# Kernel optimization log

Measured on AMD Instinct MI355X. Metric: run time of the kernel, lower is better.

## Reference

```python
import jax, jax.numpy as jnp
import numpy as np

N_NODES = 100000
N_EDGES = 1600000
IN_CH = 128
NHIDDEN = 64
OUT_CH = 40
NLAYERS = 4
ALPHA = 0.1


def setup_inputs() -> dict:
    key = jax.random.key(0)
    ks = jax.random.split(key, 7)
    x = jax.random.normal(ks[0], (N_NODES, IN_CH), dtype=jnp.float32)
    edge_index = jax.random.randint(ks[1], (2, N_EDGES), 0, N_NODES, dtype=jnp.int64)
    batch_graph = jnp.zeros((N_NODES,), dtype=jnp.int64)
    fc1_w = jax.random.normal(ks[2], (NHIDDEN, IN_CH), dtype=jnp.float32) * (1.0 / np.sqrt(IN_CH))
    fc1_b = jax.random.normal(ks[3], (NHIDDEN,), dtype=jnp.float32) * 0.01
    conv_w = jax.random.normal(ks[4], (NLAYERS, NHIDDEN, NHIDDEN), dtype=jnp.float32) * (1.0 / np.sqrt(NHIDDEN))
    fc2_w = jax.random.normal(ks[5], (OUT_CH, NHIDDEN), dtype=jnp.float32) * (1.0 / np.sqrt(NHIDDEN))
    fc2_b = jax.random.normal(ks[6], (OUT_CH,), dtype=jnp.float32) * 0.01
    return {"x": x, "edge_index": edge_index, "batch_graph": batch_graph,
            "fc1_w": fc1_w, "fc1_b": fc1_b, "conv_w": conv_w,
            "fc2_w": fc2_w, "fc2_b": fc2_b}


def reference(x, edge_index, batch_graph, fc1_w, fc1_b, conv_w, fc2_w, fc2_b):
    # eval mode: dropout layers are identity
    n = x.shape[0]
    row, col = edge_index[0], edge_index[1]  # source, target

    # gcn_norm with add_self_loops=False: sym deg^-1/2 normalization
    deg = jax.ops.segment_sum(jnp.ones_like(row, dtype=x.dtype), col, num_segments=n)
    dinv = jnp.where(deg > 0, deg ** -0.5, 0.0)
    norm = (dinv[row] * dinv[col])[:, None]  # [E, 1]

    h = jax.nn.relu(x @ fc1_w.T + fc1_b)  # [N, nhidden]
    h0 = h
    nlayers = conv_w.shape[0]
    for i in range(nlayers):
        # GCN2Conv: aggregate, initial-residual mix, weight1 matmul (beta=1)
        agg = jax.ops.segment_sum(h[row] * norm, col, num_segments=n)
        mixed = (1.0 - ALPHA) * agg + ALPHA * h0
        h = jax.nn.relu(mixed @ conv_w[i])
    out = h @ fc2_w.T + fc2_b  # [N, out_channels]
    return out
```

## Files before the change

### kernel.cpp

```cpp
#include <hip/hip_runtime.h>
#include <hip/hip_fp16.h>

#define N_NODES 100000
#define N_EDGES 1600000
#define IN_CH   128
#define NHID    64
#define OUT_CH  40
#define NBLK    391
#define NBUCK   196
#define BCAP    8960
#define ECAP    1024


__global__ __launch_bounds__(256) void k_scan1(const int* __restrict__ cnt,
                                               int* __restrict__ rowptr,
                                               int* __restrict__ bsum) {
    __shared__ int s[256];
    int t = threadIdx.x;
    int n = blockIdx.x * 256 + t;
    int v = (n < N_NODES) ? cnt[n] : 0;
    s[t] = v;
    __syncthreads();
    for (int off = 1; off < 256; off <<= 1) {
        int add = (t >= off) ? s[t - off] : 0;
        __syncthreads();
        s[t] += add;
        __syncthreads();
    }
    int incl = s[t];
    if (n < N_NODES) rowptr[n] = incl - v;
    if (t == 255) bsum[blockIdx.x] = incl;
}

__global__ __launch_bounds__(512) void k_scan2(int* __restrict__ bsum) {
    __shared__ int s[512];
    int t = threadIdx.x;
    int v = (t < NBLK) ? bsum[t] : 0;
    s[t] = v;
    __syncthreads();
    for (int off = 1; off < 512; off <<= 1) {
        int add = (t >= off) ? s[t - off] : 0;
        __syncthreads();
        s[t] += add;
        __syncthreads();
    }
    if (t < NBLK) bsum[t] = s[t] - v;
}

__global__ __launch_bounds__(256) void k_scan3(const int* __restrict__ cnt,
                                               const int* __restrict__ bsum,
                                               int* __restrict__ rowptr,
                                               float* __restrict__ dinv) {
    int n = blockIdx.x * 256 + threadIdx.x;
    if (n < N_NODES) {
        int rp = rowptr[n] + bsum[n >> 8];
        rowptr[n] = rp;
        int c = cnt[n];
        dinv[n] = (c > 0) ? rsqrtf((float)c) : 0.0f;
    }
    if (blockIdx.x == 0 && threadIdx.x == 0) rowptr[N_NODES] = N_EDGES;
}


__global__ __launch_bounds__(256) void k_scatA(const int* __restrict__ ei,
                                               int* __restrict__ bucketCnt,
                                               int2* __restrict__ ebufA) {
    __shared__ int hist[NBUCK];
    __shared__ int base[NBUCK];
    int t = threadIdx.x;
    int chunk = blockIdx.x * 4096;
    for (int i = t; i < NBUCK; i += 256) hist[i] = 0;
    __syncthreads();
#pragma unroll 4
    for (int i = 0; i < 16; i++) {
        int e = chunk + i * 256 + t;
        if (e < N_EDGES) atomicAdd(&hist[ei[N_EDGES + e] >> 9], 1);
    }
    __syncthreads();
    for (int b = t; b < NBUCK; b += 256) {
        int h = hist[b];
        base[b] = h ? atomicAdd(&bucketCnt[b], h) : 0;
    }
    __syncthreads();
#pragma unroll 4
    for (int i = 0; i < 16; i++) {
        int e = chunk + i * 256 + t;
        if (e < N_EDGES) {
            int r = ei[e], c = ei[N_EDGES + e];
            int pos = atomicAdd(&base[c >> 9], 1);
            ebufA[(size_t)(c >> 9) * BCAP + pos] = make_int2(r, c);
        }
    }
}


__global__ __launch_bounds__(256) void k_deg(const int2* __restrict__ ebufA,
                                             const int* __restrict__ bucketCnt,
                                             int* __restrict__ cnt) {
    __shared__ int hist[512];
    int b = blockIdx.x;
    int nodeB = b * 512;
    int t = threadIdx.x;
    for (int i = t; i < 512; i += 256) hist[i] = 0;
    __syncthreads();
    int nE = bucketCnt[b];
    const int2* src = ebufA + (size_t)b * BCAP;
    for (int i = t; i < nE; i += 256) atomicAdd(&hist[src[i].y - nodeB], 1);
    __syncthreads();
    for (int i = t; i < 512; i += 256) {
        int node = nodeB + i;
        if (node < N_NODES) cnt[node] = hist[i];
    }
}


__global__ __launch_bounds__(256) void k_scatB(const int2* __restrict__ ebufA,
                                               const int* __restrict__ bucketCnt,
                                               const float* __restrict__ dinv,
                                               const int* __restrict__ rowptr,
                                               int2* __restrict__ e8) {
    __shared__ int lcur[512];
    int b = blockIdx.x;
    int nodeB = b * 512;
    int t = threadIdx.x;
    for (int i = t; i < 512; i += 256) {
        int node = nodeB + i;
        lcur[i] = (node < N_NODES) ? rowptr[node] : 0;
    }
    __syncthreads();
    int nE = bucketCnt[b];
    const int2* src = ebufA + (size_t)b * BCAP;
    for (int i = t; i < nE; i += 256) {
        int2 rc = src[i];
        float w = dinv[rc.x] * dinv[rc.y];
        int pos = atomicAdd(&lcur[rc.y - nodeB], 1);
        e8[pos] = make_int2(rc.x, __float_as_int(w));
    }
}

__device__ __forceinline__ void store_h4(__half* dst, float a, float b, float c, float d) {
    union { uint2 u; __half2 h[2]; } pk;
    pk.h[0] = __floats2half2_rn(a, b);
    pk.h[1] = __floats2half2_rn(c, d);
    *(uint2*)dst = pk.u;
}


__global__ __launch_bounds__(256, 4) void k_fc1(const float* __restrict__ x,
                                                const float* __restrict__ w,
                                                const float* __restrict__ b,
                                                __half* __restrict__ h016) {
    __shared__ float xs[64 * 128];
    int t = threadIdx.x;
    int nodeBase = blockIdx.x * 64;

    {
        int lane8 = t & 7, rhalf = t >> 3;
#pragma unroll
        for (int r2 = 0; r2 < 2; r2++) {
            int nl = r2 * 32 + rhalf;
            int n = nodeBase + nl;
            int swz = (nl ^ (nl >> 3)) & 7;
            float4* dstrow = (float4*)(xs + nl * 128);
            if (n < N_NODES) {
                const float4* src = (const float4*)(x + (size_t)n * IN_CH);
#pragma unroll
                for (int q = 0; q < 4; q++) dstrow[(q * 8 + lane8) ^ swz] = src[q * 8 + lane8];
            } else {
                float4 z = {0.f, 0.f, 0.f, 0.f};
#pragma unroll
                for (int q = 0; q < 4; q++) dstrow[(q * 8 + lane8) ^ swz] = z;
            }
        }
    }
    __syncthreads();

    int tx = t & 15, ty = t >> 4;
    int n0 = tx * 4, o0 = ty * 4;
    int swz0 = ((n0 + 0) ^ ((n0 + 0) >> 3)) & 7;
    int swz1 = ((n0 + 1) ^ ((n0 + 1) >> 3)) & 7;
    int swz2 = ((n0 + 2) ^ ((n0 + 2) >> 3)) & 7;
    int swz3 = ((n0 + 3) ^ ((n0 + 3) >> 3)) & 7;
    const float4* xrow0 = (const float4*)(xs + (n0 + 0) * 128);
    const float4* xrow1 = (const float4*)(xs + (n0 + 1) * 128);
    const float4* xrow2 = (const float4*)(xs + (n0 + 2) * 128);
    const float4* xrow3 = (const float4*)(xs + (n0 + 3) * 128);

    float c[4][4];
#pragma unroll
    for (int i = 0; i < 4; i++)
#pragma unroll
        for (int j = 0; j < 4; j++) c[i][j] = 0.f;

#pragma unroll 4
    for (int k = 0; k < IN_CH; k += 4) {
        int kk = k >> 2;
        float4 b0 = *(const float4*)&w[(size_t)(o0 + 0) * IN_CH + k];
        float4 b1 = *(const float4*)&w[(size_t)(o0 + 1) * IN_CH + k];
        float4 b2 = *(const float4*)&w[(size_t)(o0 + 2) * IN_CH + k];
        float4 b3 = *(const float4*)&w[(size_t)(o0 + 3) * IN_CH + k];
        float4 a0 = xrow0[kk ^ swz0];
        float4 a1 = xrow1[kk ^ swz1];
        float4 a2 = xrow2[kk ^ swz2];
        float4 a3 = xrow3[kk ^ swz3];
#pragma unroll
        for (int i = 0; i < 4; i++) {
            float4 a = (i == 0) ? a0 : (i == 1) ? a1 : (i == 2) ? a2 : a3;
            c[i][0] = fmaf(a.x, b0.x, fmaf(a.y, b0.y, fmaf(a.z, b0.z, fmaf(a.w, b0.w, c[i][0]))));
            c[i][1] = fmaf(a.x, b1.x, fmaf(a.y, b1.y, fmaf(a.z, b1.z, fmaf(a.w, b1.w, c[i][1]))));
            c[i][2] = fmaf(a.x, b2.x, fmaf(a.y, b2.y, fmaf(a.z, b2.z, fmaf(a.w, b2.w, c[i][2]))));
            c[i][3] = fmaf(a.x, b3.x, fmaf(a.y, b3.y, fmaf(a.z, b3.z, fmaf(a.w, b3.w, c[i][3]))));
        }
    }

    float4 bias = *(const float4*)&b[o0];
#pragma unroll
    for (int i = 0; i < 4; i++) {
        int n = nodeBase + n0 + i;
        if (n < N_NODES) {
            store_h4(&h016[(size_t)n * NHID + o0],
                     fmaxf(c[i][0] + bias.x, 0.f), fmaxf(c[i][1] + bias.y, 0.f),
                     fmaxf(c[i][2] + bias.z, 0.f), fmaxf(c[i][3] + bias.w, 0.f));
        }
    }
}


__global__ __launch_bounds__(256, 4) void k_conv(const __half* __restrict__ hin,
                                                 const __half* __restrict__ h0f16,
                                                 const int* __restrict__ rowptr,
                                                 const int2* __restrict__ e8,
                                                 const float* __restrict__ W,
                                                 __half* __restrict__ hout) {
    __shared__ int2  eS[ECAP];
    __shared__ float mix[32 * 68];
    int t = threadIdx.x;
    int nodeBase = blockIdx.x * 32;
    int grp = t >> 3;
    int cg = (t & 7) * 8;

    int base0 = rowptr[nodeBase];
    int nE = rowptr[nodeBase + 32] - base0;
    int nStage = (nE < ECAP) ? nE : ECAP;
    for (int i = t; i < nStage; i += 256) eS[i] = e8[base0 + i];

    int n = nodeBase + grp;
    int s = rowptr[n], e = rowptr[n + 1];
    int d = e - s;
    int hi = (d > 0) ? (e - 1) : 0;
    __syncthreads();

    float acc[8];
#pragma unroll
    for (int i = 0; i < 8; i++) acc[i] = 0.f;

#define LOADM(pm, jb)                                                    \
    {                                                                    \
        _Pragma("unroll")                                                \
        for (int u = 0; u < 4; u++) {                                    \
            int idx = min((jb) + u, hi);                                 \
            int li = idx - base0;                                        \
            if (li < ECAP) pm[u] = eS[li];                               \
            else           pm[u] = e8[idx];                              \
        }                                                                \
    }
#define ISSUE(pv, pm)                                                    \
    {                                                                    \
        _Pragma("unroll")                                                \
        for (int u = 0; u < 4; u++)                                      \
            pv[u] = *(const float4*)&hin[(size_t)pm[u].x * NHID + cg];   \
    }
#define FMA4(pm, pv, jb)                                                 \
    {                                                                    \
        _Pragma("unroll")                                                \
        for (int u = 0; u < 4; u++) {                                    \
            float wgt = ((jb) + u < e) ? __int_as_float(pm[u].y) : 0.f;  \
            const __half* hp = (const __half*)&pv[u];                    \
            _Pragma("unroll")                                            \
            for (int q = 0; q < 8; q++)                                  \
                acc[q] = fmaf(wgt, __half2float(hp[q]), acc[q]);         \
        }                                                                \
    }

    int2  pmA[4], pmB[4], pmC[4];
    float4 pvA[4], pvB[4], pvC[4];
    if (d > 0) {
        LOADM(pmA, s);     ISSUE(pvA, pmA);
        LOADM(pmB, s + 4); ISSUE(pvB, pmB);
        LOADM(pmC, s + 8); ISSUE(pvC, pmC);
    }

    for (int j = s; j < e; j += 12) {
        {
            FMA4(pmA, pvA, j);
            int jn = j + 12;
            if (jn < e) { LOADM(pmA, jn); ISSUE(pvA, pmA); }
        }
        if (j + 4 < e) {
            FMA4(pmB, pvB, j + 4);
            int jn = j + 16;
            if (jn < e) { LOADM(pmB, jn); ISSUE(pvB, pmB); }
        }
        if (j + 8 < e) {
            FMA4(pmC, pvC, j + 8);
            int jn = j + 20;
            if (jn < e) { LOADM(pmC, jn); ISSUE(pvC, pmC); }
        }
    }
#undef LOADM
#undef ISSUE
#undef FMA4

    {
        float4 raw = *(const float4*)&h0f16[(size_t)n * NHID + cg];
        const __half* h0h = (const __half*)&raw;
        float m[8];
#pragma unroll
        for (int q = 0; q < 8; q++)
            m[q] = fmaf(0.9f, acc[q], 0.1f * __half2float(h0h[q]));
        float4 m0 = {m[0], m[1], m[2], m[3]};
        float4 m1 = {m[4], m[5], m[6], m[7]};
        *(float4*)&mix[grp * 68 + cg] = m0;
        *(float4*)&mix[grp * 68 + cg + 4] = m1;
    }
    __syncthreads();

    int tx = t & 15, ty = t >> 4;
    int o0 = tx * 4, r0 = ty * 2;
    float c[2][4];
#pragma unroll
    for (int i = 0; i < 2; i++)
#pragma unroll
        for (int j = 0; j < 4; j++) c[i][j] = 0.f;

#pragma unroll 4
    for (int k = 0; k < NHID; k += 4) {
        float4 b0 = *(const float4*)&W[(k + 0) * NHID + o0];
        float4 b1 = *(const float4*)&W[(k + 1) * NHID + o0];
        float4 b2 = *(const float4*)&W[(k + 2) * NHID + o0];
        float4 b3 = *(const float4*)&W[(k + 3) * NHID + o0];
#pragma unroll
        for (int i = 0; i < 2; i++) {
            float4 a = *(const float4*)&mix[(r0 + i) * 68 + k];
            c[i][0] = fmaf(a.x, b0.x, fmaf(a.y, b1.x, fmaf(a.z, b2.x, fmaf(a.w, b3.x, c[i][0]))));
            c[i][1] = fmaf(a.x, b0.y, fmaf(a.y, b1.y, fmaf(a.z, b2.y, fmaf(a.w, b3.y, c[i][1]))));
            c[i][2] = fmaf(a.x, b0.z, fmaf(a.y, b1.z, fmaf(a.z, b2.z, fmaf(a.w, b3.z, c[i][2]))));
            c[i][3] = fmaf(a.x, b0.w, fmaf(a.y, b1.w, fmaf(a.z, b2.w, fmaf(a.w, b3.w, c[i][3]))));
        }
    }
#pragma unroll
    for (int i = 0; i < 2; i++) {
        int n2 = nodeBase + r0 + i;
        store_h4(&hout[(size_t)n2 * NHID + o0],
                 fmaxf(c[i][0], 0.f), fmaxf(c[i][1], 0.f),
                 fmaxf(c[i][2], 0.f), fmaxf(c[i][3], 0.f));
    }
}


__global__ __launch_bounds__(256) void k_fc2(const __half* __restrict__ h,
                                             const float* __restrict__ w,
                                             const float* __restrict__ b,
                                             float* __restrict__ out) {
    __shared__ float wT[NHID * 44];
    __shared__ float hs[64 * 68];
    int t = threadIdx.x;
    int nodeBase = blockIdx.x * 64;

    for (int id = t; id < NHID * OUT_CH; id += 256) {
        int o = id >> 6, k = id & 63;
        wT[k * 44 + o] = w[id];
    }
    {
        int nl = t >> 2, seg = t & 3;
        int n = nodeBase + nl;
        float* dst = hs + nl * 68 + seg * 16;
        if (n < N_NODES) {
            float4 raw0 = *(const float4*)&h[(size_t)n * NHID + seg * 16];
            float4 raw1 = *(const float4*)&h[(size_t)n * NHID + seg * 16 + 8];
            const __half2* hp0 = (const __half2*)&raw0;
            const __half2* hp1 = (const __half2*)&raw1;
#pragma unroll
            for (int q = 0; q < 4; q++) {
                float2 f = __half22float2(hp0[q]);
                dst[q * 2 + 0] = f.x;
                dst[q * 2 + 1] = f.y;
            }
#pragma unroll
            for (int q = 0; q < 4; q++) {
                float2 f = __half22float2(hp1[q]);
                dst[8 + q * 2 + 0] = f.x;
                dst[8 + q * 2 + 1] = f.y;
            }
        } else {
#pragma unroll
            for (int q = 0; q < 16; q++) dst[q] = 0.f;
        }
    }
    __syncthreads();

    if (t < 160) {
        int tx = t % 10, ty = t / 10;
        int o0 = tx * 4, n0 = ty * 4;
        float c[4][4];
#pragma unroll
        for (int i = 0; i < 4; i++)
#pragma unroll
            for (int j = 0; j < 4; j++) c[i][j] = 0.f;

#pragma unroll 4
        for (int k = 0; k < NHID; k += 4) {
            float4 b0 = *(const float4*)&wT[(k + 0) * 44 + o0];
            float4 b1 = *(const float4*)&wT[(k + 1) * 44 + o0];
            float4 b2 = *(const float4*)&wT[(k + 2) * 44 + o0];
            float4 b3 = *(const float4*)&wT[(k + 3) * 44 + o0];
#pragma unroll
            for (int i = 0; i < 4; i++) {
                float4 a = *(const float4*)&hs[(n0 + i) * 68 + k];
                c[i][0] = fmaf(a.x, b0.x, fmaf(a.y, b1.x, fmaf(a.z, b2.x, fmaf(a.w, b3.x, c[i][0]))));
                c[i][1] = fmaf(a.x, b0.y, fmaf(a.y, b1.y, fmaf(a.z, b2.y, fmaf(a.w, b3.y, c[i][1]))));
                c[i][2] = fmaf(a.x, b0.z, fmaf(a.y, b1.z, fmaf(a.z, b2.z, fmaf(a.w, b3.z, c[i][2]))));
                c[i][3] = fmaf(a.x, b0.w, fmaf(a.y, b1.w, fmaf(a.z, b2.w, fmaf(a.w, b3.w, c[i][3]))));
            }
        }
        float4 bias = *(const float4*)&b[o0];
#pragma unroll
        for (int i = 0; i < 4; i++) {
            int n = nodeBase + n0 + i;
            if (n < N_NODES) {
                float4 v;
                v.x = c[i][0] + bias.x;
                v.y = c[i][1] + bias.y;
                v.z = c[i][2] + bias.z;
                v.w = c[i][3] + bias.w;
                *(float4*)&out[(size_t)n * OUT_CH + o0] = v;
            }
        }
    }
}


extern "C" void kernel_launch(void* const* d_in, const int* in_sizes, int n_in,
                              void* d_out, int out_size, void* d_ws, size_t ws_size,
                              hipStream_t stream) {
    const float* x    = (const float*)d_in[0];
    const int*   ei   = (const int*)d_in[1];
    const float* fc1w = (const float*)d_in[3];
    const float* fc1b = (const float*)d_in[4];
    const float* cw   = (const float*)d_in[5];
    const float* fc2w = (const float*)d_in[6];
    const float* fc2b = (const float*)d_in[7];
    float* out = (float*)d_out;

    char* p = (char*)d_ws;
    auto alloc = [&](size_t bytes) { char* r = p; p += (bytes + 255) & ~(size_t)255; return r; };
    __half* h016   = (__half*)alloc((size_t)N_NODES * NHID * 2);
    __half* ha16   = (__half*)alloc((size_t)N_NODES * NHID * 2);
    __half* hb16   = (__half*)alloc((size_t)N_NODES * NHID * 2);
    int2*   e8     = (int2*)  alloc(((size_t)N_EDGES + 8) * 8);
    int2*   ebufA  = (int2*)  alloc((size_t)NBUCK * BCAP * 8);
    int*    cnt    = (int*)   alloc((size_t)N_NODES * 4);
    int*    rowptr = (int*)   alloc((size_t)(N_NODES + 1) * 4);
    int*    bCnt   = (int*)   alloc((size_t)NBUCK * 4);
    float*  dinv   = (float*) alloc((size_t)N_NODES * 4);
    int*    bsum   = (int*)   alloc(512 * 4);

    hipMemsetAsync(bCnt, 0, (size_t)NBUCK * 4, stream);
    k_scatA<<<(N_EDGES + 4095) / 4096, 256, 0, stream>>>(ei, bCnt, ebufA);
    k_deg  <<<NBUCK, 256, 0, stream>>>(ebufA, bCnt, cnt);
    k_scan1<<<NBLK, 256, 0, stream>>>(cnt, rowptr, bsum);
    k_scan2<<<1, 512, 0, stream>>>(bsum);
    k_scan3<<<NBLK, 256, 0, stream>>>(cnt, bsum, rowptr, dinv);
    k_scatB<<<NBUCK, 256, 0, stream>>>(ebufA, bCnt, dinv, rowptr, e8);

    int gb64 = (N_NODES + 63) / 64;
    int gb32 = N_NODES / 32;
    k_fc1 <<<gb64, 256, 0, stream>>>(x, fc1w, fc1b, h016);
    k_conv<<<gb32, 256, 0, stream>>>(h016, h016, rowptr, e8, cw + 0 * NHID * NHID, ha16);
    k_conv<<<gb32, 256, 0, stream>>>(ha16, h016, rowptr, e8, cw + 1 * NHID * NHID, hb16);
    k_conv<<<gb32, 256, 0, stream>>>(hb16, h016, rowptr, e8, cw + 2 * NHID * NHID, ha16);
    k_conv<<<gb32, 256, 0, stream>>>(ha16, h016, rowptr, e8, cw + 3 * NHID * NHID, hb16);
    k_fc2 <<<gb64, 256, 0, stream>>>(hb16, fc2w, fc2b, out);
}
```

Measured before the change: 425.1 us.

## Factor symmetric norm into node scaling and store 4-byte edge indices

Rewrites the normalized aggregation as dinv[dst] times the sum of pre-scaled features, so each node's output is pre-multiplied by dinv[src] when written. Edges then store only the source index (4 bytes instead of 8), and the inner loop becomes plain adds, with padded lanes pointing at a zeroed sentinel row. The prefetch depth drops from three batches of four to two. This halves edge-list traffic and removes per-edge multiplies, but adds an extra fp16 rounding of the scaled features and reuses the bucket buffer for the final layer's output.

New measurement: 441.7 us. +3.9%, slower.

```diff
diff --git a/kernel.cpp b/kernel.cpp
--- a/kernel.cpp
+++ b/kernel.cpp
@@ -116,9 +116,8 @@
 
 __global__ __launch_bounds__(256) void k_scatB(const int2* __restrict__ ebufA,
                                                const int* __restrict__ bucketCnt,
-                                               const float* __restrict__ dinv,
                                                const int* __restrict__ rowptr,
-                                               int2* __restrict__ e8) {
+                                               int* __restrict__ e4) {
     __shared__ int lcur[512];
     int b = blockIdx.x;
     int nodeB = b * 512;
@@ -132,9 +131,8 @@
     const int2* src = ebufA + (size_t)b * BCAP;
     for (int i = t; i < nE; i += 256) {
         int2 rc = src[i];
-        float w = dinv[rc.x] * dinv[rc.y];
         int pos = atomicAdd(&lcur[rc.y - nodeB], 1);
-        e8[pos] = make_int2(rc.x, __float_as_int(w));
+        e4[pos] = rc.x;
     }
 }
 
@@ -149,7 +147,9 @@
 __global__ __launch_bounds__(256, 4) void k_fc1(const float* __restrict__ x,
                                                 const float* __restrict__ w,
                                                 const float* __restrict__ b,
-                                                __half* __restrict__ h016) {
+                                                const float* __restrict__ dinv,
+                                                __half* __restrict__ h016,
+                                                __half* __restrict__ hs1) {
     __shared__ float xs[64 * 128];
     int t = threadIdx.x;
     int nodeBase = blockIdx.x * 64;
@@ -218,106 +218,125 @@
     for (int i = 0; i < 4; i++) {
         int n = nodeBase + n0 + i;
         if (n < N_NODES) {
-            store_h4(&h016[(size_t)n * NHID + o0],
-                     fmaxf(c[i][0] + bias.x, 0.f), fmaxf(c[i][1] + bias.y, 0.f),
-                     fmaxf(c[i][2] + bias.z, 0.f), fmaxf(c[i][3] + bias.w, 0.f));
-        }
-    }
-}
-
-
-__global__ __launch_bounds__(256, 4) void k_conv(const __half* __restrict__ hin,
-                                                 const __half* __restrict__ h0f16,
+            float vx = fmaxf(c[i][0] + bias.x, 0.f);
+            float vy = fmaxf(c[i][1] + bias.y, 0.f);
+            float vz = fmaxf(c[i][2] + bias.z, 0.f);
+            float vw = fmaxf(c[i][3] + bias.w, 0.f);
+            store_h4(&h016[(size_t)n * NHID + o0], vx, vy, vz, vw);
+            float dn = dinv[n];
+            store_h4(&hs1[(size_t)n * NHID + o0], vx * dn, vy * dn, vz * dn, vw * dn);
+        }
+    }
+}
+
+
+__global__ __launch_bounds__(256, 4) void k_conv(const __half* __restrict__ hs,
+                                                 const __half* __restrict__ h0,
                                                  const int* __restrict__ rowptr,
-                                                 const int2* __restrict__ e8,
+                                                 const int* __restrict__ e4,
                                                  const float* __restrict__ W,
-                                                 __half* __restrict__ hout) {
-    __shared__ int2  eS[ECAP];
+                                                 const float* __restrict__ dinv,
+                                                 __half* __restrict__ hout,
+                                                 int scaled) {
+    __shared__ int   eS[ECAP];
     __shared__ float mix[32 * 68];
     int t = threadIdx.x;
     int nodeBase = blockIdx.x * 32;
     int grp = t >> 3;
     int cg = (t & 7) * 8;
 
+    int n = nodeBase + grp;
+    int s = rowptr[n], e = rowptr[n + 1];
     int base0 = rowptr[nodeBase];
     int nE = rowptr[nodeBase + 32] - base0;
     int nStage = (nE < ECAP) ? nE : ECAP;
-    for (int i = t; i < nStage; i += 256) eS[i] = e8[base0 + i];
-
-    int n = nodeBase + grp;
-    int s = rowptr[n], e = rowptr[n + 1];
-    int d = e - s;
-    int hi = (d > 0) ? (e - 1) : 0;
-    __syncthreads();
-
-    float acc[8];
-#pragma unroll
-    for (int i = 0; i < 8; i++) acc[i] = 0.f;
-
+    for (int i = t; i < nStage; i += 256) eS[i] = e4[base0 + i];
+
+#define LOADM_G(pm, jb)                                                  \
+    {                                                                    \
+        _Pragma("unroll")                                                \
+        for (int u = 0; u < 4; u++) {                                    \
+            int idx = (jb) + u;                                          \
+            pm[u] = (idx < e) ? e4[idx] : N_NODES;                       \
+        }                                                                \
+    }
 #define LOADM(pm, jb)                                                    \
     {                                                                    \
         _Pragma("unroll")                                                \
         for (int u = 0; u < 4; u++) {                                    \
-            int idx = min((jb) + u, hi);                                 \
-            int li = idx - base0;                                        \
-            if (li < ECAP) pm[u] = eS[li];                               \
-            else           pm[u] = e8[idx];                              \
+            int idx = (jb) + u;                                          \
+            int m = N_NODES;                                             \
+            if (idx < e) {                                               \
+                int li = idx - base0;                                    \
+                m = (li < ECAP) ? eS[li] : e4[idx];                      \
+            }                                                            \
+            pm[u] = m;                                                   \
         }                                                                \
     }
 #define ISSUE(pv, pm)                                                    \
     {                                                                    \
         _Pragma("unroll")                                                \
         for (int u = 0; u < 4; u++)                                      \
-            pv[u] = *(const float4*)&hin[(size_t)pm[u].x * NHID + cg];   \
-    }
-#define FMA4(pm, pv, jb)                                                 \
+            pv[u] = *(const float4*)&hs[(size_t)pm[u] * NHID + cg];      \
+    }
+#define ACC4(cv)                                                         \
     {                                                                    \
         _Pragma("unroll")                                                \
         for (int u = 0; u < 4; u++) {                                    \
-            float wgt = ((jb) + u < e) ? __int_as_float(pm[u].y) : 0.f;  \
-            const __half* hp = (const __half*)&pv[u];                    \
+            const __half2* hp = (const __half2*)&cv[u];                  \
             _Pragma("unroll")                                            \
-            for (int q = 0; q < 8; q++)                                  \
-                acc[q] = fmaf(wgt, __half2float(hp[q]), acc[q]);         \
+            for (int q = 0; q < 4; q++) {                                \
+                float2 f = __half22float2(hp[q]);                        \
+                acc[q * 2 + 0] += f.x;                                   \
+                acc[q * 2 + 1] += f.y;                                   \
+            }                                                            \
         }                                                                \
     }
 
-    int2  pmA[4], pmB[4], pmC[4];
-    float4 pvA[4], pvB[4], pvC[4];
-    if (d > 0) {
-        LOADM(pmA, s);     ISSUE(pvA, pmA);
-        LOADM(pmB, s + 4); ISSUE(pvB, pmB);
-        LOADM(pmC, s + 8); ISSUE(pvC, pmC);
-    }
-
-    for (int j = s; j < e; j += 12) {
+    int    pmA[4], pmB[4];
+    float4 pvA[4], pvB[4];
+    LOADM_G(pmA, s);     ISSUE(pvA, pmA);
+    LOADM_G(pmB, s + 4); ISSUE(pvB, pmB);
+
+    float dn = dinv[n];
+    float4 h0raw = *(const float4*)&h0[(size_t)n * NHID + cg];
+
+    float acc[8];
+#pragma unroll
+    for (int i = 0; i < 8; i++) acc[i] = 0.f;
+
+    __syncthreads();
+
+    for (int j = s; j < e; j += 8) {
         {
-            FMA4(pmA, pvA, j);
+            float4 cv[4];
+#pragma unroll
+            for (int u = 0; u < 4; u++) cv[u] = pvA[u];
+            int jn = j + 8;
+            if (jn < e) { LOADM(pmA, jn); ISSUE(pvA, pmA); }
+            ACC4(cv);
+        }
+        if (j + 4 < e) {
+            float4 cv[4];
+#pragma unroll
+            for (int u = 0; u < 4; u++) cv[u] = pvB[u];
             int jn = j + 12;
-            if (jn < e) { LOADM(pmA, jn); ISSUE(pvA, pmA); }
-        }
-        if (j + 4 < e) {
-            FMA4(pmB, pvB, j + 4);
-            int jn = j + 16;
             if (jn < e) { LOADM(pmB, jn); ISSUE(pvB, pmB); }
-        }
-        if (j + 8 < e) {
-            FMA4(pmC, pvC, j + 8);
-            int jn = j + 20;
-            if (jn < e) { LOADM(pmC, jn); ISSUE(pvC, pmC); }
-        }
-    }
+            ACC4(cv);
+        }
+    }
+#undef LOADM_G
 #undef LOADM
 #undef ISSUE
-#undef FMA4
+#undef ACC4
 
     {
-        float4 raw = *(const float4*)&h0f16[(size_t)n * NHID + cg];
-        const __half* h0h = (const __half*)&raw;
+        const __half* h0h = (const __half*)&h0raw;
+        float a = 0.9f * dn;
         float m[8];
 #pragma unroll
         for (int q = 0; q < 8; q++)
-            m[q] = fmaf(0.9f, acc[q], 0.1f * __half2float(h0h[q]));
+            m[q] = fmaf(a, acc[q], 0.1f * __half2float(h0h[q]));
         float4 m0 = {m[0], m[1], m[2], m[3]};
         float4 m1 = {m[4], m[5], m[6], m[7]};
         *(float4*)&mix[grp * 68 + cg] = m0;
@@ -351,9 +370,11 @@
 #pragma unroll
     for (int i = 0; i < 2; i++) {
         int n2 = nodeBase + r0 + i;
+        float sc = 1.0f;
+        if (scaled) sc = dinv[n2];
         store_h4(&hout[(size_t)n2 * NHID + o0],
-                 fmaxf(c[i][0], 0.f), fmaxf(c[i][1], 0.f),
-                 fmaxf(c[i][2], 0.f), fmaxf(c[i][3], 0.f));
+                 fmaxf(c[i][0], 0.f) * sc, fmaxf(c[i][1], 0.f) * sc,
+                 fmaxf(c[i][2], 0.f) * sc, fmaxf(c[i][3], 0.f) * sc);
     }
 }
 
@@ -455,30 +476,34 @@
     char* p = (char*)d_ws;
     auto alloc = [&](size_t bytes) { char* r = p; p += (bytes + 255) & ~(size_t)255; return r; };
     __half* h016   = (__half*)alloc((size_t)N_NODES * NHID * 2);
-    __half* ha16   = (__half*)alloc((size_t)N_NODES * NHID * 2);
-    __half* hb16   = (__half*)alloc((size_t)N_NODES * NHID * 2);
-    int2*   e8     = (int2*)  alloc(((size_t)N_EDGES + 8) * 8);
+    __half* hsA    = (__half*)alloc((size_t)(N_NODES + 1) * NHID * 2);
+    __half* hsB    = (__half*)alloc((size_t)(N_NODES + 1) * NHID * 2);
+    int*    e4     = (int*)   alloc((size_t)(N_EDGES + 8) * 4);
     int2*   ebufA  = (int2*)  alloc((size_t)NBUCK * BCAP * 8);
     int*    cnt    = (int*)   alloc((size_t)N_NODES * 4);
     int*    rowptr = (int*)   alloc((size_t)(N_NODES + 1) * 4);
     int*    bCnt   = (int*)   alloc((size_t)NBUCK * 4);
     float*  dinv   = (float*) alloc((size_t)N_NODES * 4);
     int*    bsum   = (int*)   alloc(512 * 4);
+    __half* h4     = (__half*)ebufA;
 
     hipMemsetAsync(bCnt, 0, (size_t)NBUCK * 4, stream);
+    hipMemsetAsync(hsA + (size_t)N_NODES * NHID, 0, NHID * 2, stream);
+    hipMemsetAsync(hsB + (size_t)N_NODES * NHID, 0, NHID * 2, stream);
+
     k_scatA<<<(N_EDGES + 4095) / 4096, 256, 0, stream>>>(ei, bCnt, ebufA);
     k_deg  <<<NBUCK, 256, 0, stream>>>(ebufA, bCnt, cnt);
     k_scan1<<<NBLK, 256, 0, stream>>>(cnt, rowptr, bsum);
     k_scan2<<<1, 512, 0, stream>>>(bsum);
     k_scan3<<<NBLK, 256, 0, stream>>>(cnt, bsum, rowptr, dinv);
-    k_scatB<<<NBUCK, 256, 0, stream>>>(ebufA, bCnt, dinv, rowptr, e8);
+    k_scatB<<<NBUCK, 256, 0, stream>>>(ebufA, bCnt, rowptr, e4);
 
     int gb64 = (N_NODES + 63) / 64;
     int gb32 = N_NODES / 32;
-    k_fc1 <<<gb64, 256, 0, stream>>>(x, fc1w, fc1b, h016);
-    k_conv<<<gb32, 256, 0, stream>>>(h016, h016, rowptr, e8, cw + 0 * NHID * NHID, ha16);
-    k_conv<<<gb32, 256, 0, stream>>>(ha16, h016, rowptr, e8, cw + 1 * NHID * NHID, hb16);
-    k_conv<<<gb32, 256, 0, stream>>>(hb16, h016, rowptr, e8, cw + 2 * NHID * NHID, ha16);
-    k_conv<<<gb32, 256, 0, stream>>>(ha16, h016, rowptr, e8, cw + 3 * NHID * NHID, hb16);
-    k_fc2 <<<gb64, 256, 0, stream>>>(hb16, fc2w, fc2b, out);
-}
+    k_fc1 <<<gb64, 256, 0, stream>>>(x, fc1w, fc1b, dinv, h016, hsA);
+    k_conv<<<gb32, 256, 0, stream>>>(hsA, h016, rowptr, e4, cw + 0 * NHID * NHID, dinv, hsB, 1);
+    k_conv<<<gb32, 256, 0, stream>>>(hsB, h016, rowptr, e4, cw + 1 * NHID * NHID, dinv, hsA, 1);
+    k_conv<<<gb32, 256, 0, stream>>>(hsA, h016, rowptr, e4, cw + 2 * NHID * NHID, dinv, hsB, 1);
+    k_conv<<<gb32, 256, 0, stream>>>(hsB, h016, rowptr, e4, cw + 3 * NHID * NHID, dinv, h4, 0);
+    k_fc2 <<<gb64, 256, 0, stream>>>(h4, fc2w, fc2b, out);
+}
```
